# Kernel tuning notes

Hardware: AMD Instinct MI355X
Metric: run time of the kernel (lower is better)

The kernel has to match this reference:

```python
import jax, jax.numpy as jnp
import numpy as np

NUM_HEADS = 12


def setup_inputs() -> dict:
    key = jax.random.key(0)
    ks = jax.random.split(key, 6)
    B, N, C = 2, 1569, 768  # N = 1 + num_frames * seq_len = 1 + 8*196
    s = 0.02
    return {
        "x": jax.random.normal(ks[0], (B, N, C), jnp.float32),
        "W_qkv": jax.random.normal(ks[1], (C, 3 * C), jnp.float32) * s,
        "W_pq": jax.random.normal(ks[2], (C, C), jnp.float32) * s,
        "W_pkv": jax.random.normal(ks[3], (C, 2 * C), jnp.float32) * s,
        "W_proj": jax.random.normal(ks[4], (C, C), jnp.float32) * s,
        "b_proj": jax.random.normal(ks[5], (C,), jnp.float32) * s,
        "seq_len": 196,
        "num_frames": 8,
    }


def reference(x, W_qkv, W_pq, W_pkv, W_proj, b_proj, seq_len, num_frames):
    h = NUM_HEADS
    B, N, C = x.shape
    d = C // h
    P, F = seq_len, num_frames  # N == 1 + F*P
    S = F * P
    scale = d ** (-0.5)

    # qkv projection (no bias), split heads -> (B*h, N, d)
    qkv = x @ W_qkv
    q, k, v = jnp.split(qkv, 3, axis=-1)

    def heads(t):
        return t.reshape(B, N, h, d).transpose(0, 2, 1, 3).reshape(B * h, N, d)

    q, k, v = map(heads, (q, k, v))

    # --- CLS token: plain attention over all tokens ---
    cls_sim = jnp.einsum('bid,bjd->bij', q[:, :1] * scale, k)  # (B*h,1,N)
    cls_attn = jax.nn.softmax(cls_sim, axis=-1)
    cls_out = jnp.einsum('bij,bjd->bid', cls_attn, v)  # (B*h,1,d)
    cls_out = cls_out.reshape(B, h, 1, d).transpose(0, 2, 1, 3).reshape(B, 1, C)

    # --- Stage 1: space attention (softmax over patches n within each frame f) ---
    q_, k_, v_ = q[:, 1:], k[:, 1:], v[:, 1:]  # (B*h, S, d)
    q_dot_k = jnp.einsum('bqd,bnd->bqn', q_, k_).reshape(B * h, S, F, P)
    space_attn = jax.nn.softmax(scale * q_dot_k, axis=-1)  # (B*h, S, F, P)
    v4 = v_.reshape(B * h, F, P, d)
    traj = jnp.einsum('bqfn,bfnd->bqfd', space_attn, v4)  # (B*h, S, F, d)
    # merge heads into channels: (B, S, F, C)
    traj = traj.reshape(B, h, S, F, d).transpose(0, 2, 3, 1, 4).reshape(B, S, F, C)

    # --- Diagonal gather: token s=f*P+n takes its own-frame trajectory f ---
    fidx = jnp.repeat(jnp.arange(F), P)  # (S,)
    x_diag = jnp.take_along_axis(traj, fidx[None, :, None, None], axis=2)[:, :, 0, :]  # (B,S,C)

    # --- Stage 2: temporal attention over frames f ---
    q2 = (x_diag @ W_pq).reshape(B, S, h, d).transpose(0, 2, 1, 3) * scale  # (B,h,S,d)
    kv2 = traj @ W_pkv  # (B,S,F,2C)
    k2, v2 = jnp.split(kv2, 2, axis=-1)

    def heads5(t):  # (B,S,F,C) -> (B,h,S,F,d)
        return t.reshape(B, S, F, h, d).transpose(0, 3, 1, 2, 4)

    k2 = heads5(k2)
    attn = jax.nn.softmax(jnp.einsum('bhsd,bhsfd->bhsf', q2, k2), axis=-1)  # (B,h,S,F)
    # use_original_code=True: values are the trajectory tensor itself, not v2
    xv = heads5(traj)
    out = jnp.einsum('bhsf,bhsfd->bhsd', attn, xv)  # (B,h,S,d)
    out = out.transpose(0, 2, 1, 3).reshape(B, S, C)

    out = jnp.concatenate([cls_out, out], axis=1) @ W_proj + b_proj  # (B,N,C)
    return out, attn
```

## Files before the change

### kernel.cpp

```cpp
#include <hip/hip_runtime.h>

#define B_ 2
#define N_ 1569
#define C_ 768
#define H_ 12
#define D_ 64
#define P_ 196
#define F_ 8
#define S_ 1568
#define QKVLD 2304
#define SCALE 0.125f

typedef unsigned short ushort_t;
using short8 = __attribute__((ext_vector_type(8))) short;
using f32x4  = __attribute__((ext_vector_type(4))) float;

__device__ __forceinline__ ushort_t f2bf(float x) {
    unsigned u = __float_as_uint(x);
    u += 0x7fffu + ((u >> 16) & 1);
    return (ushort_t)(u >> 16);
}
__device__ __forceinline__ float bf2f(ushort_t h) {
    return __uint_as_float((unsigned)h << 16);
}
__device__ __forceinline__ uint2 pack4(float a, float b, float c, float d) {
    uint2 o;
    o.x = f2bf(a) | ((unsigned)f2bf(b) << 16);
    o.y = f2bf(c) | ((unsigned)f2bf(d) << 16);
    return o;
}

__global__ __launch_bounds__(256)
void cvt_f32_bf16(const float* __restrict__ s, ushort_t* __restrict__ d, int n4)
{
    int i = blockIdx.x * 256 + threadIdx.x;
    if (i < n4) {
        float4 v = ((const float4*)s)[i];
        ((uint2*)d)[i] = pack4(v.x, v.y, v.z, v.w);
    }
}

__global__ __launch_bounds__(256)
void transpose_cvt(const float* __restrict__ src, ushort_t* __restrict__ dst,
                   int K, int ldsrc)
{
    __shared__ float tle[32][33];
    const int n0 = blockIdx.x * 32, k0 = blockIdx.y * 32;
    const int tx = threadIdx.x & 31, ty = threadIdx.x >> 5;
#pragma unroll
    for (int j = 0; j < 4; j++)
        tle[ty + 8 * j][tx] = src[(long)(k0 + ty + 8 * j) * ldsrc + n0 + tx];
    __syncthreads();
#pragma unroll
    for (int j = 0; j < 4; j++)
        dst[(long)(n0 + ty + 8 * j) * K + k0 + tx] = f2bf(tle[tx][ty + 8 * j]);
}

template<int GATHER, int OUTBF>
__global__ __launch_bounds__(256)
void gemm_bf16(const ushort_t* __restrict__ A, const ushort_t* __restrict__ Bt,
               void* __restrict__ Cv, int M, int Nn, int K,
               float alpha, const float* __restrict__ bias)
{
    __shared__ ushort_t As[128][32];
    __shared__ ushort_t Bs[128][32];

    const int tid = threadIdx.x;
    const int m0 = blockIdx.x * 128, n0 = blockIdx.y * 128;
    const int wave = tid >> 6, lane = tid & 63;
    const int wm = (wave & 1) * 64, wn = (wave >> 1) * 64;
    const int lrow = lane & 15, quad = lane >> 4;

    const int srow = tid >> 2, sseg = tid & 3;
    int ma0 = m0 + srow;      if (ma0 >= M) ma0 = M - 1;
    int ma1 = m0 + 64 + srow; if (ma1 >= M) ma1 = M - 1;
    long ra0, ra1;
    if (GATHER) {
        ra0 = (long)ma0 * F_ + (ma0 % S_) / P_;
        ra1 = (long)ma1 * F_ + (ma1 % S_) / P_;
    } else { ra0 = ma0; ra1 = ma1; }
    const ushort_t* ap0 = A + ra0 * K + sseg * 8;
    const ushort_t* ap1 = A + ra1 * K + sseg * 8;
    const ushort_t* bp0 = Bt + (long)(n0 + srow) * K + sseg * 8;
    const ushort_t* bp1 = Bt + (long)(n0 + 64 + srow) * K + sseg * 8;

    f32x4 acc[4][4];
#pragma unroll
    for (int i = 0; i < 4; i++)
#pragma unroll
        for (int j = 0; j < 4; j++) acc[i][j] = (f32x4){0.f, 0.f, 0.f, 0.f};

    uint4 aV0 = *(const uint4*)ap0;
    uint4 aV1 = *(const uint4*)ap1;
    uint4 bV0 = *(const uint4*)bp0;
    uint4 bV1 = *(const uint4*)bp1;

    const int nk = K >> 5;
    for (int kt = 0; kt < nk; kt++) {
        __syncthreads();
        *(uint4*)&As[srow][sseg * 8]      = aV0;
        *(uint4*)&As[64 + srow][sseg * 8] = aV1;
        *(uint4*)&Bs[srow][sseg * 8]      = bV0;
        *(uint4*)&Bs[64 + srow][sseg * 8] = bV1;
        __syncthreads();
        if (kt + 1 < nk) {
            int k0 = (kt + 1) * 32;
            aV0 = *(const uint4*)(ap0 + k0);
            aV1 = *(const uint4*)(ap1 + k0);
            bV0 = *(const uint4*)(bp0 + k0);
            bV1 = *(const uint4*)(bp1 + k0);
        }
        short8 af[4], bf[4];
#pragma unroll
        for (int mt = 0; mt < 4; mt++)
            af[mt] = *(const short8*)&As[wm + mt * 16 + lrow][quad * 8];
#pragma unroll
        for (int nt = 0; nt < 4; nt++)
            bf[nt] = *(const short8*)&Bs[wn + nt * 16 + lrow][quad * 8];
#pragma unroll
        for (int mt = 0; mt < 4; mt++)
#pragma unroll
            for (int nt = 0; nt < 4; nt++)
                acc[mt][nt] = __builtin_amdgcn_mfma_f32_16x16x32_bf16(
                    af[mt], bf[nt], acc[mt][nt], 0, 0, 0);
    }

#pragma unroll
    for (int mt = 0; mt < 4; mt++) {
#pragma unroll
        for (int nt = 0; nt < 4; nt++) {
            int row = m0 + wm + mt * 16 + quad * 4;
            int col = n0 + wn + nt * 16 + lrow;
            float bv = bias ? bias[col] : 0.f;
#pragma unroll
            for (int r = 0; r < 4; r++) {
                if (row + r < M) {
                    float v = acc[mt][nt][r] * alpha + bv;
                    if (OUTBF)
                        ((ushort_t*)Cv)[(long)(row + r) * Nn + col] = f2bf(v);
                    else
                        ((float*)Cv)[(long)(row + r) * Nn + col] = v;
                }
            }
        }
    }
}

__global__ __launch_bounds__(256)
void prep_kv(const float* __restrict__ qkv, ushort_t* __restrict__ q_bf,
             ushort_t* __restrict__ k_bf, ushort_t* __restrict__ vT_bf)
{
    const int f = blockIdx.x, h = blockIdx.y, b = blockIdx.z;
    const int t = threadIdx.x;
    const long rowbase = (long)(b * N_ + 1 + f * P_) * QKVLD;

    {
        ushort_t* qd = q_bf + ((long)(b * H_ + h) * S_ + f * P_) * 64;
        for (int u = t; u < P_ * 16; u += 256) {
            int row = u >> 4, seg = u & 15;
            float4 v = *(const float4*)(qkv + rowbase + (long)row * QKVLD + h * 64 + seg * 4);
            *(uint2*)(qd + (long)row * 64 + seg * 4) = pack4(v.x, v.y, v.z, v.w);
        }
    }
    {
        ushort_t* kd = k_bf + (long)((b * H_ + h) * F_ + f) * 13312;
        for (int u = t; u < 208 * 16; u += 256) {
            int key = u >> 4, seg = u & 15;
            float4 v = make_float4(0.f, 0.f, 0.f, 0.f);
            if (key < P_)
                v = *(const float4*)(qkv + rowbase + (long)key * QKVLD + 768 + h * 64 + seg * 4);
            int ks = seg >> 3, qq = (seg >> 1) & 3, j0 = (seg & 1) * 4;
            int nt = key >> 4, lr = key & 15;
            *(uint2*)(kd + ((ks * 13 + nt) * 64 + qq * 16 + lr) * 8 + j0)
                = pack4(v.x, v.y, v.z, v.w);
        }
    }
    __shared__ float Vl[224][68];
    for (int u = t; u < 224 * 16; u += 256) {
        int key = u >> 4, seg = u & 15;
        float4 v = make_float4(0.f, 0.f, 0.f, 0.f);
        if (key < P_)
            v = *(const float4*)(qkv + rowbase + (long)key * QKVLD + 1536 + h * 64 + seg * 4);
        *(float4*)&Vl[key][seg * 4] = v;
    }
    __syncthreads();
    {
        ushort_t* vd = vT_bf + (long)((b * H_ + h) * F_ + f) * 14336;
        for (int u = t; u < 64 * 56; u += 256) {
            int d = u / 56, kb = u % 56;
            int s = kb >> 3, qq = (kb >> 1) & 3, j0 = (kb & 1) * 4;
            int nt = d >> 4, lr = d & 15;
            *(uint2*)(vd + ((s * 4 + nt) * 64 + qq * 16 + lr) * 8 + j0) =
                pack4(Vl[kb*4+0][d], Vl[kb*4+1][d], Vl[kb*4+2][d], Vl[kb*4+3][d]);
        }
    }
}

__global__ __launch_bounds__(256)
void traj_attn_mfma(const ushort_t* __restrict__ q_bf,
                    const ushort_t* __restrict__ k_bf,
                    const ushort_t* __restrict__ vT_bf,
                    ushort_t* __restrict__ traj)
{
    __shared__ __align__(16) ushort_t Pl[4][7 * 512];

    const int t = threadIdx.x;
    const int wave = t >> 6, lane = t & 63;
    const int lrow = lane & 15, quad = lane >> 4;
    const int qt = blockIdx.x, h = blockIdx.y, b = blockIdx.z;
    const int s0 = qt * 64;
    const bool v12 = (lrow < 4);

    int qrow = s0 + wave * 16 + lrow; if (qrow > S_ - 1) qrow = S_ - 1;
    const ushort_t* qp = q_bf + ((long)(b * H_ + h) * S_ + qrow) * 64 + quad * 8;
    short8 a0 = *(const short8*)qp;
    short8 a1 = *(const short8*)(qp + 32);

    *(uint2*)&Pl[wave][6 * 512 + 256 + lane * 4] = (uint2){0, 0};

    const ushort_t* kfb = k_bf  + (long)((b * H_ + h) * F_) * 13312;
    const ushort_t* vfb = vT_bf + (long)((b * H_ + h) * F_) * 14336;

#pragma unroll 1
    for (int f = 0; f < F_; f++) {
        const ushort_t* kf = kfb + (long)f * 13312;
        const ushort_t* vf = vfb + (long)f * 14336;

        f32x4 acc[13];
#pragma unroll
        for (int nt = 0; nt < 13; nt++) acc[nt] = (f32x4){0.f, 0.f, 0.f, 0.f};
#pragma unroll
        for (int nt = 0; nt < 13; nt++) {
            short8 bv = *(const short8*)(kf + (long)nt * 512 + lane * 8);
            acc[nt] = __builtin_amdgcn_mfma_f32_16x16x32_bf16(a0, bv, acc[nt], 0, 0, 0);
        }
#pragma unroll
        for (int nt = 0; nt < 13; nt++) {
            short8 bv = *(const short8*)(kf + (long)(13 + nt) * 512 + lane * 8);
            acc[nt] = __builtin_amdgcn_mfma_f32_16x16x32_bf16(a1, bv, acc[nt], 0, 0, 0);
        }

        float rl[4];
#pragma unroll
        for (int r = 0; r < 4; r++) {
            float mx = acc[0][r];
#pragma unroll
            for (int nt = 1; nt < 12; nt++) mx = fmaxf(mx, acc[nt][r]);
            if (v12) mx = fmaxf(mx, acc[12][r]);
#pragma unroll
            for (int off = 1; off < 16; off <<= 1)
                mx = fmaxf(mx, __shfl_xor(mx, off, 16));
            float sum = 0.f;
#pragma unroll
            for (int nt = 0; nt < 12; nt++) {
                float w = __expf((acc[nt][r] - mx) * SCALE);
                acc[nt][r] = w; sum += w;
            }
            {
                float w = v12 ? __expf((acc[12][r] - mx) * SCALE) : 0.f;
                acc[12][r] = w; sum += w;
            }
#pragma unroll
            for (int off = 1; off < 16; off <<= 1)
                sum += __shfl_xor(sum, off, 16);
            rl[r] = 1.f / sum;
        }

#pragma unroll
        for (int nt = 0; nt < 13; nt++) {
            int key = nt * 16 + lrow;
            int base = (key >> 5) * 512 + ((key >> 3) & 3) * 128 + (key & 7) + quad * 32;
#pragma unroll
            for (int r = 0; r < 4; r++)
                Pl[wave][base + r * 8] = f2bf(acc[nt][r]);
        }
        asm volatile("s_waitcnt lgkmcnt(0)" ::: "memory");

        f32x4 av[4];
#pragma unroll
        for (int nt = 0; nt < 4; nt++) av[nt] = (f32x4){0.f, 0.f, 0.f, 0.f};
#pragma unroll
        for (int s = 0; s < 7; s++) {
            short8 af = *(const short8*)&Pl[wave][s * 512 + lane * 8];
#pragma unroll
            for (int nt = 0; nt < 4; nt++) {
                short8 bv = *(const short8*)(vf + (long)(s * 4 + nt) * 512 + lane * 8);
                av[nt] = __builtin_amdgcn_mfma_f32_16x16x32_bf16(af, bv, av[nt], 0, 0, 0);
            }
        }

#pragma unroll
        for (int nt = 0; nt < 4; nt++)
#pragma unroll
            for (int r = 0; r < 4; r++) {
                int so = s0 + wave * 16 + quad * 4 + r;
                if (so < S_)
                    traj[((long)(b * S_ + so) * F_ + f) * C_ + h * 64 + nt * 16 + lrow]
                        = f2bf(av[nt][r] * rl[r]);
            }
    }
}

#define CLS_CH 13
__global__ __launch_bounds__(256)
void cls_attn_part(const float* __restrict__ qkv, float* __restrict__ part)
{
    const int c = blockIdx.x, hh = blockIdx.y, b = blockIdx.z;
    const int t = threadIdx.x;
    const int n0 = c * 128;
    const int nk = (N_ - n0 < 128) ? (N_ - n0) : 128;

    __shared__ float qs[64];
    __shared__ float sc[128];
    __shared__ float red[256];

    if (t < 64) qs[t] = qkv[(long)(b * N_) * QKVLD + hh * 64 + t];
    __syncthreads();

    if (t < 128) {
        float acc = -1e30f;
        if (t < nk) {
            const float* krow = qkv + (long)(b * N_ + n0 + t) * QKVLD + 768 + hh * 64;
            acc = 0.f;
#pragma unroll
            for (int j4 = 0; j4 < 16; j4++) {
                float4 kv = *(const float4*)(krow + j4 * 4);
                acc = fmaf(kv.x, qs[j4*4+0], acc);
                acc = fmaf(kv.y, qs[j4*4+1], acc);
                acc = fmaf(kv.z, qs[j4*4+2], acc);
                acc = fmaf(kv.w, qs[j4*4+3], acc);
            }
            acc *= SCALE;
        }
        sc[t] = acc;
        red[t] = acc;
    }
    __syncthreads();
    for (int s = 64; s > 0; s >>= 1) {
        if (t < s && t + s < 128) red[t] = fmaxf(red[t], red[t + s]);
        __syncthreads();
    }
    const float m = red[0];
    __syncthreads();

    if (t < 128) {
        float w = (t < nk) ? __expf(sc[t] - m) : 0.f;
        sc[t] = w;
        red[t] = w;
    }
    __syncthreads();
    for (int s = 64; s > 0; s >>= 1) {
        if (t < s && t + s < 128) red[t] += red[t + s];
        __syncthreads();
    }
    const float lsum = red[0];
    __syncthreads();

    const int j = t & 63, grp = t >> 6;
    float acc = 0.f;
    for (int n = grp; n < nk; n += 4)
        acc = fmaf(sc[n], qkv[(long)(b * N_ + n0 + n) * QKVLD + 1536 + hh * 64 + j], acc);
    red[t] = acc;
    __syncthreads();

    float* pp = part + (long)(((b * H_ + hh) * CLS_CH) + c) * 68;
    if (t < 64)
        pp[2 + t] = red[t] + red[64 + t] + red[128 + t] + red[192 + t];
    if (t == 0) { pp[0] = m; pp[1] = lsum; }
}

__global__ __launch_bounds__(64)
void cls_attn_merge(const float* __restrict__ part, float* __restrict__ outcat)
{
    const int bh = blockIdx.x;
    const int b = bh / H_, hh = bh % H_;
    const int t = threadIdx.x;
    const float* pp = part + (long)(bh * CLS_CH) * 68;

    float m = -1e30f;
#pragma unroll
    for (int c = 0; c < CLS_CH; c++) m = fmaxf(m, pp[c * 68]);
    float l = 0.f, o = 0.f;
#pragma unroll
    for (int c = 0; c < CLS_CH; c++) {
        float w = __expf(pp[c * 68] - m);
        l = fmaf(pp[c * 68 + 1], w, l);
        o = fmaf(pp[c * 68 + 2 + t], w, o);
    }
    outcat[(long)(b * N_) * C_ + hh * 64 + t] = o / l;
}

__global__ __launch_bounds__(256)
void attn2_kernel(const float* __restrict__ q2, const ushort_t* __restrict__ k2,
                  const ushort_t* __restrict__ traj, float* __restrict__ outcat,
                  float* __restrict__ attn_out)
{
    const int bs = blockIdx.x;
    const int b = bs / S_, s = bs % S_;
    __shared__ float qs[768];
    __shared__ ushort_t ks[8 * 768];
    __shared__ float logit[12][8];
    __shared__ float wsm[12][8];
    const int t = threadIdx.x;

    const float* qrow = q2 + (long)bs * 768;
    if (t < 192) *(float4*)&qs[t * 4] = *(const float4*)(qrow + t * 4);
    const uint4* krow = (const uint4*)(k2 + (long)bs * 6144);
#pragma unroll
    for (int u = t; u < 768; u += 256)
        *(uint4*)&ks[u * 8] = krow[u];
    __syncthreads();

    if (t < 96) {
        int hh = t >> 3, f = t & 7;
        float acc = 0.f;
#pragma unroll 8
        for (int j = 0; j < 64; j++)
            acc = fmaf(qs[hh * 64 + j], bf2f(ks[f * 768 + hh * 64 + j]), acc);
        logit[hh][f] = acc;
    }
    __syncthreads();
    if (t < 12) {
        float m = logit[t][0];
#pragma unroll
        for (int f = 1; f < 8; f++) m = fmaxf(m, logit[t][f]);
        float w[8], sum = 0.f;
#pragma unroll
        for (int f = 0; f < 8; f++) { w[f] = __expf(logit[t][f] - m); sum += w[f]; }
        float r = 1.f / sum;
#pragma unroll
        for (int f = 0; f < 8; f++) wsm[t][f] = w[f] * r;
    }
    __syncthreads();
    if (t < 96) {
        int hh = t >> 3, f = t & 7;
        attn_out[((long)(b * H_ + hh) * S_ + s) * 8 + f] = wsm[hh][f];
    }
    if (t < 96) {
        const int c0 = t * 8, hh = t >> 3;
        const ushort_t* trow = traj + (long)bs * 6144;
        float o[8];
#pragma unroll
        for (int i = 0; i < 8; i++) o[i] = 0.f;
#pragma unroll
        for (int f = 0; f < 8; f++) {
            uint4 tv = *(const uint4*)(trow + f * 768 + c0);
            float wv = wsm[hh][f];
            const ushort_t* e = (const ushort_t*)&tv;
#pragma unroll
            for (int i = 0; i < 8; i++) o[i] = fmaf(wv, bf2f(e[i]), o[i]);
        }
        float* orow = outcat + ((long)(b * N_) + 1 + s) * 768 + c0;
        *(float4*)orow       = make_float4(o[0], o[1], o[2], o[3]);
        *(float4*)(orow + 4) = make_float4(o[4], o[5], o[6], o[7]);
    }
}

extern "C" void kernel_launch(void* const* d_in, const int* in_sizes, int n_in,
                              void* d_out, int out_size, void* d_ws, size_t ws_size,
                              hipStream_t stream)
{
    (void)in_sizes; (void)n_in; (void)out_size; (void)ws_size;
    const float* x     = (const float*)d_in[0];
    const float* Wqkv  = (const float*)d_in[1];
    const float* Wpq   = (const float*)d_in[2];
    const float* Wpkv  = (const float*)d_in[3];
    const float* Wproj = (const float*)d_in[4];
    const float* bproj = (const float*)d_in[5];
    float* out = (float*)d_out;

    char* p = (char*)d_ws;
    float*    qkv     = (float*)p;
    ushort_t* traj_bf = (ushort_t*)p;
    p += (size_t)25088 * 768 * 2;
    float* q2 = (float*)p;  p += (size_t)3136 * 768 * 4;
    char* c0 = p;
    ushort_t* k2_bf = (ushort_t*)c0;
    ushort_t* x_bf  = (ushort_t*)c0;
    ushort_t* q_bf  = (ushort_t*)(c0 + (size_t)4819968);
    ushort_t* k_bf  = (ushort_t*)(c0 + (size_t)4819968 + 4816896);
    ushort_t* vT_bf = (ushort_t*)(c0 + (size_t)4819968 + 4816896 + 5111808);
    p += (size_t)25088 * 768 * 2;
    float*    outcat    = (float*)p;     p += (size_t)3138 * 768 * 4;
    ushort_t* outcat_bf = (ushort_t*)p;  p += (size_t)3138 * 768 * 2;
    ushort_t* Wqkv_t  = (ushort_t*)p;    p += (size_t)1769472 * 2;
    ushort_t* Wpq_t   = (ushort_t*)p;    p += (size_t)589824 * 2;
    ushort_t* Wpkv_t  = (ushort_t*)p;    p += (size_t)589824 * 2;
    ushort_t* Wproj_t = (ushort_t*)p;    p += (size_t)589824 * 2;
    float*    cls_part = (float*)p;      p += (size_t)24 * CLS_CH * 68 * 4;
    float* attn_out = out + (size_t)3138 * 768;

    cvt_f32_bf16<<<2354, 256, 0, stream>>>(x, x_bf, 602496);
    transpose_cvt<<<dim3(72, 24), 256, 0, stream>>>(Wqkv,  Wqkv_t,  768, 2304);
    transpose_cvt<<<dim3(24, 24), 256, 0, stream>>>(Wpq,   Wpq_t,   768, 768);
    transpose_cvt<<<dim3(24, 24), 256, 0, stream>>>(Wpkv,  Wpkv_t,  768, 1536);
    transpose_cvt<<<dim3(24, 24), 256, 0, stream>>>(Wproj, Wproj_t, 768, 768);

    gemm_bf16<0, 0><<<dim3(25, 18), 256, 0, stream>>>(x_bf, Wqkv_t, qkv, 3138, 2304, 768, 1.f, nullptr);
    prep_kv<<<dim3(8, 12, 2), 256, 0, stream>>>(qkv, q_bf, k_bf, vT_bf);
    cls_attn_part<<<dim3(CLS_CH, 12, 2), 256, 0, stream>>>(qkv, cls_part);
    cls_attn_merge<<<24, 64, 0, stream>>>(cls_part, outcat);
    traj_attn_mfma<<<dim3(25, 12, 2), 256, 0, stream>>>(q_bf, k_bf, vT_bf, traj_bf);
    gemm_bf16<1, 0><<<dim3(25, 6), 256, 0, stream>>>(traj_bf, Wpq_t, q2, 3136, 768, 768, SCALE, nullptr);
    gemm_bf16<0, 1><<<dim3(196, 6), 256, 0, stream>>>(traj_bf, Wpkv_t, k2_bf, 25088, 768, 768, 1.f, nullptr);
    attn2_kernel<<<3136, 256, 0, stream>>>(q2, k2_bf, traj_bf, outcat, attn_out);
    cvt_f32_bf16<<<2354, 256, 0, stream>>>(outcat, outcat_bf, 602496);
    gemm_bf16<0, 0><<<dim3(25, 6), 256, 0, stream>>>(outcat_bf, Wproj_t, out, 3138, 768, 768, 1.f, bproj);
}
```

Measured before the change: 342.3 us.

## Load GEMM tiles directly into LDS with XOR-swizzled layout

Replaces the register-staged global-to-shared copies in the bf16 GEMM with direct global_load_lds 16-byte transfers. It also XOR-swizzles the 8-element chunks within each 32-element row to reduce LDS bank conflicts on the MFMA fragment reads. The old version prefetched the next tile into registers while computing the current one. The new loop issues the loads and waits on vmcnt(0) before computing, so it loses that overlap and each tile's load latency is exposed.

```diff
diff --git a/kernel.cpp b/kernel.cpp
--- a/kernel.cpp
+++ b/kernel.cpp
@@ -12,8 +12,13 @@
 #define SCALE 0.125f
 
 typedef unsigned short ushort_t;
+typedef unsigned int u32;
+typedef __attribute__((address_space(1))) const u32 gu32;
+typedef __attribute__((address_space(3))) u32 lu32;
 using short8 = __attribute__((ext_vector_type(8))) short;
 using f32x4  = __attribute__((ext_vector_type(4))) float;
+
+#define GLD16(gp, lp) __builtin_amdgcn_global_load_lds((gu32*)(gp), (lu32*)(lp), 16, 0, 0)
 
 __device__ __forceinline__ ushort_t f2bf(float x) {
     unsigned u = __float_as_uint(x);
@@ -72,6 +77,7 @@
     const int lrow = lane & 15, quad = lane >> 4;
 
     const int srow = tid >> 2, sseg = tid & 3;
+    const int gseg = sseg ^ ((srow >> 1) & 3);
     int ma0 = m0 + srow;      if (ma0 >= M) ma0 = M - 1;
     int ma1 = m0 + 64 + srow; if (ma1 >= M) ma1 = M - 1;
     long ra0, ra1;
@@ -79,10 +85,15 @@
         ra0 = (long)ma0 * F_ + (ma0 % S_) / P_;
         ra1 = (long)ma1 * F_ + (ma1 % S_) / P_;
     } else { ra0 = ma0; ra1 = ma1; }
-    const ushort_t* ap0 = A + ra0 * K + sseg * 8;
-    const ushort_t* ap1 = A + ra1 * K + sseg * 8;
-    const ushort_t* bp0 = Bt + (long)(n0 + srow) * K + sseg * 8;
-    const ushort_t* bp1 = Bt + (long)(n0 + 64 + srow) * K + sseg * 8;
+    const ushort_t* ap0 = A + ra0 * K + gseg * 8;
+    const ushort_t* ap1 = A + ra1 * K + gseg * 8;
+    const ushort_t* bp0 = Bt + (long)(n0 + srow) * K + gseg * 8;
+    const ushort_t* bp1 = Bt + (long)(n0 + 64 + srow) * K + gseg * 8;
+
+    ushort_t* asp0 = &As[srow][sseg * 8];
+    ushort_t* asp1 = &As[64 + srow][sseg * 8];
+    ushort_t* bsp0 = &Bs[srow][sseg * 8];
+    ushort_t* bsp1 = &Bs[64 + srow][sseg * 8];
 
     f32x4 acc[4][4];
 #pragma unroll
@@ -90,33 +101,27 @@
 #pragma unroll
         for (int j = 0; j < 4; j++) acc[i][j] = (f32x4){0.f, 0.f, 0.f, 0.f};
 
-    uint4 aV0 = *(const uint4*)ap0;
-    uint4 aV1 = *(const uint4*)ap1;
-    uint4 bV0 = *(const uint4*)bp0;
-    uint4 bV1 = *(const uint4*)bp1;
+    const int rswz = (lrow >> 1) & 3;
+    const int rchunk = (quad ^ rswz) * 8;
 
     const int nk = K >> 5;
     for (int kt = 0; kt < nk; kt++) {
         __syncthreads();
-        *(uint4*)&As[srow][sseg * 8]      = aV0;
-        *(uint4*)&As[64 + srow][sseg * 8] = aV1;
-        *(uint4*)&Bs[srow][sseg * 8]      = bV0;
-        *(uint4*)&Bs[64 + srow][sseg * 8] = bV1;
+        const int k0 = kt * 32;
+        GLD16(ap0 + k0, asp0);
+        GLD16(ap1 + k0, asp1);
+        GLD16(bp0 + k0, bsp0);
+        GLD16(bp1 + k0, bsp1);
+        asm volatile("s_waitcnt vmcnt(0)" ::: "memory");
         __syncthreads();
-        if (kt + 1 < nk) {
-            int k0 = (kt + 1) * 32;
-            aV0 = *(const uint4*)(ap0 + k0);
-            aV1 = *(const uint4*)(ap1 + k0);
-            bV0 = *(const uint4*)(bp0 + k0);
-            bV1 = *(const uint4*)(bp1 + k0);
-        }
+
         short8 af[4], bf[4];
 #pragma unroll
         for (int mt = 0; mt < 4; mt++)
-            af[mt] = *(const short8*)&As[wm + mt * 16 + lrow][quad * 8];
+            af[mt] = *(const short8*)&As[wm + mt * 16 + lrow][rchunk];
 #pragma unroll
         for (int nt = 0; nt < 4; nt++)
-            bf[nt] = *(const short8*)&Bs[wn + nt * 16 + lrow][quad * 8];
+            bf[nt] = *(const short8*)&Bs[wn + nt * 16 + lrow][rchunk];
 #pragma unroll
         for (int mt = 0; mt < 4; mt++)
 #pragma unroll
```

After: 359.8 us. 5.1% more time.
